# Kernel optimization log

Measured on AMD Instinct MI355X. Metric: run time of the kernel, lower is better.

The kernel has to match this reference:

```python
import jax, jax.numpy as jnp
import numpy as np


def setup_inputs() -> dict:
    key = jax.random.key(0)
    ks = jax.random.split(key, 4)
    B, S, D, H, E = 2, 2048, 1024, 4096, 8
    scale_in = 1.0 / np.sqrt(D)
    scale_h = 1.0 / np.sqrt(H)
    return {
        "x": jax.random.normal(ks[0], (B, S, D), dtype=jnp.float32),
        "Wr": jax.random.normal(ks[1], (E, D), dtype=jnp.float32) * scale_in,
        "br": jnp.zeros((E,), dtype=jnp.float32),
        "W1": jax.random.normal(ks[2], (E, H, D), dtype=jnp.float32) * scale_in,
        "b1": jnp.zeros((E, H), dtype=jnp.float32),
        "W2": jax.random.normal(ks[3], (E, D, H), dtype=jnp.float32) * scale_h,
        "b2": jnp.zeros((E, D), dtype=jnp.float32),
        "top_k": 2,
    }


def reference(x, Wr, br, W1, b1, W2, b2, top_k):
    B, S, D = x.shape
    E = Wr.shape[0]
    x_flat = x.reshape(-1, D)                                   # [N, D]
    # Router: top-k logits, softmax over the selected k values only
    logits = x_flat @ Wr.T + br                                 # [N, E]
    top_vals, top_idx = jax.lax.top_k(logits, top_k)            # [N, k]
    gates = jax.nn.softmax(top_vals, axis=-1)                   # [N, k]
    # Per-expert combine weight: gate_e[n, e] = sum_k gates[n, k] * 1[top_idx[n,k]==e]
    gate_e = jnp.einsum("nk,nke->ne", gates,
                        jax.nn.one_hot(top_idx, E, dtype=x.dtype))  # [N, E]
    # Dense all-expert MLP (grouped GEMM), then masked combine. Same math as
    # the per-expert gather/scatter loop: unselected experts get zero gate.
    h = jax.nn.relu(jnp.einsum("nd,ehd->neh", x_flat, W1) + b1)     # [N, E, H]
    y = jnp.einsum("neh,edh->ned", h, W2) + b2                      # [N, E, D]
    out = jnp.einsum("ned,ne->nd", y, gate_e)                       # [N, D]
    return out.reshape(B, S, D)
```

## Files before the change

### kernel.cpp

```cpp
#include <hip/hip_runtime.h>
#include <hip/hip_bf16.h>
#include <stdint.h>

#define N_TOK 4096
#define D_ 1024
#define H_ 4096
#define E_ 8
#define NSLOT (N_TOK*2)
#define BM 128
#define BN 128
#define BK 32
#define MAXT 72
#define BM2 256
#define BN2 256
#define BK2 32
#define MAXT2 40

typedef __attribute__((ext_vector_type(8))) short short8;
typedef __attribute__((ext_vector_type(4))) float floatx4;
typedef unsigned int u32;

__device__ __forceinline__ unsigned short f2bf(float f){
    union { float f; unsigned int u; } c; c.f = f;
    unsigned int u = c.u;
    unsigned int r = (u + 0x7fffu + ((u >> 16) & 1u)) >> 16;
    return (unsigned short)r;
}

__device__ __forceinline__ void async16(const void* g, void* l){
    __builtin_amdgcn_global_load_lds(
        (const __attribute__((address_space(1))) u32*)g,
        (__attribute__((address_space(3))) u32*)l, 16, 0, 0);
}

__device__ __forceinline__ void sb(){ __builtin_amdgcn_sched_barrier(0); }
__device__ __forceinline__ void barrier_only(){ sb(); __builtin_amdgcn_s_barrier(); sb(); }

__global__ __launch_bounds__(256) void cvt_kernel(
    const float* __restrict__ src, unsigned short* __restrict__ dst, int n4)
{
    int stride = gridDim.x * 256;
    for (int i = blockIdx.x * 256 + threadIdx.x; i < n4; i += stride){
        float4 v = ((const float4*)src)[i];
        ushort4 o; o.x=f2bf(v.x); o.y=f2bf(v.y); o.z=f2bf(v.z); o.w=f2bf(v.w);
        ((ushort4*)dst)[i] = o;
    }
}

__global__ __launch_bounds__(256) void router_kernel(
    const float* __restrict__ x, const float* __restrict__ Wr,
    const float* __restrict__ br, int* __restrict__ topIdx,
    float* __restrict__ topGate)
{
    int n = blockIdx.x * 4 + (threadIdx.x >> 6);
    int lane = threadIdx.x & 63;
    const float4* xp = (const float4*)(x + (size_t)n * D_);
    float acc[E_];
#pragma unroll
    for (int e = 0; e < E_; e++) acc[e] = 0.f;
#pragma unroll
    for (int j = 0; j < 4; j++){
        int idx = j * 64 + lane;
        float4 xv = xp[idx];
#pragma unroll
        for (int e = 0; e < E_; e++){
            float4 wv = ((const float4*)(Wr + (size_t)e * D_))[idx];
            acc[e] += xv.x*wv.x + xv.y*wv.y + xv.z*wv.z + xv.w*wv.w;
        }
    }
#pragma unroll
    for (int e = 0; e < E_; e++){
        float v = acc[e];
        for (int off = 32; off > 0; off >>= 1) v += __shfl_xor(v, off, 64);
        acc[e] = v;
    }
    if (lane == 0){
        float best = -1e30f, second = -1e30f; int bi = 0, si = 0;
#pragma unroll
        for (int e = 0; e < E_; e++){
            float v = acc[e] + br[e];
            if (v > best){ second = best; si = bi; best = v; bi = e; }
            else if (v > second){ second = v; si = e; }
        }
        float e1 = __expf(second - best);
        float denom = 1.f + e1;
        topIdx[n*2+0] = bi;  topIdx[n*2+1] = si;
        topGate[n*2+0] = 1.f/denom;  topGate[n*2+1] = e1/denom;
    }
}

__global__ __launch_bounds__(256) void hist_kernel(
    const int* __restrict__ topIdx, int* __restrict__ hdr)
{
    __shared__ int c[E_];
    int t = threadIdx.x;
    if (t < E_) c[t] = 0;
    __syncthreads();
    int e = topIdx[blockIdx.x * 256 + t];
    atomicAdd(&c[e], 1);
    __syncthreads();
    if (t < E_) hdr[256 + blockIdx.x * E_ + t] = c[t];
}

__global__ __launch_bounds__(64) void scan2_kernel(int* __restrict__ hdr)
{
    __shared__ int cnt[32 * E_];
    __shared__ int tot[E_];
    __shared__ int offs[E_ + 1];
    int t = threadIdx.x;
    for (int i = t; i < 32 * E_; i += 64) cnt[i] = hdr[256 + i];
    __syncthreads();
    if (t < E_){
        int s = 0;
        for (int b = 0; b < 32; b++) s += cnt[b * E_ + t];
        tot[t] = s;
    }
    __syncthreads();
    if (t == 0){
        int o = 0;
        for (int e = 0; e < E_; e++){ offs[e] = o; o += tot[e]; }
        offs[E_] = o;
    }
    __syncthreads();
    if (t < E_ + 1) hdr[16 + t] = offs[t];
    if (t < E_){
        int run = offs[t];
        for (int b = 0; b < 32; b++){ hdr[512 + b * E_ + t] = run; run += cnt[b * E_ + t]; }
    }
    if (t == 0){
        int tn = 0;
        for (int e = 0; e < E_; e++){
            int nt = (tot[e] + BM - 1) >> 7;
            for (int i = 0; i < nt; i++){ hdr[32 + tn] = e; hdr[112 + tn] = offs[e] + (i << 7); tn++; }
        }
        for (; tn < MAXT; tn++){ hdr[32 + tn] = -1; hdr[112 + tn] = 0; }
        int t2 = 0;
        for (int e = 0; e < E_; e++){
            int nt = (tot[e] + BM2 - 1) >> 8;
            for (int i = 0; i < nt; i++){ hdr[768 + t2] = e; hdr[808 + t2] = offs[e] + (i << 8); t2++; }
        }
        for (; t2 < MAXT2; t2++){ hdr[768 + t2] = -1; hdr[808 + t2] = 0; }
    }
}

__global__ __launch_bounds__(256) void pos_kernel(
    const int* __restrict__ topIdx, const float* __restrict__ topGate,
    const int* __restrict__ hdr, int* __restrict__ posOf,
    int* __restrict__ rowTok, float* __restrict__ rowGate)
{
    __shared__ int c[E_];
    int t = threadIdx.x;
    if (t < E_) c[t] = 0;
    __syncthreads();
    int slot = blockIdx.x * 256 + t;
    int e = topIdx[slot];
    int r = atomicAdd(&c[e], 1);
    int pos = hdr[512 + blockIdx.x * E_ + e] + r;
    posOf[slot] = pos;
    rowTok[pos] = slot >> 1;
    rowGate[pos] = topGate[slot];
}

__global__ __launch_bounds__(256) void copy_kernel(
    const float* __restrict__ x, const int* __restrict__ posOf,
    unsigned short* __restrict__ xg)
{
    int slot = blockIdx.x * 4 + (threadIdx.x >> 6);
    int lane = threadIdx.x & 63;
    int n = slot >> 1;
    int pos = posOf[slot];
    const float4* xp = (const float4*)(x + (size_t)n * D_);
    ushort4* op = (ushort4*)(xg + (size_t)pos * D_);
#pragma unroll
    for (int j = 0; j < 4; j++){
        float4 v = xp[j * 64 + lane];
        ushort4 o; o.x=f2bf(v.x); o.y=f2bf(v.y); o.z=f2bf(v.z); o.w=f2bf(v.w);
        op[j * 64 + lane] = o;
    }
}

template<int MODE>
__global__ __launch_bounds__(512, 2) void moe_gemm2(
    const unsigned short* __restrict__ A, int Ktot,
    const unsigned short* __restrict__ Wbase, size_t wStride,
    const float* __restrict__ biasBase, int biasStride,
    const int* __restrict__ hdr,
    const int* __restrict__ rowTok, const float* __restrict__ rowGate,
    unsigned short* __restrict__ hout, float* __restrict__ out)
{
    int nwg  = gridDim.x * gridDim.y * gridDim.z;
    int orig = (blockIdx.z * gridDim.y + blockIdx.y) * gridDim.x + blockIdx.x;
    int xcd = orig & 7, loc = orig >> 3;
    int q8 = nwg >> 3, r8 = nwg & 7;
    int wgid = (xcd < r8 ? xcd * (q8 + 1) : r8 * (q8 + 1) + (xcd - r8) * q8) + loc;
    int bx = wgid % gridDim.x;
    int tt = wgid / gridDim.x;
    int by = tt % gridDim.y;
    int bz = tt / gridDim.y;

    int e = hdr[768 + bx];
    if (e < 0) return;
    int rowBase = hdr[808 + bx];
    int validRows = hdr[16 + e + 1] - rowBase;

    int kChunk = Ktot / gridDim.z;
    int kStart = bz * kChunk;
    int nIter  = kChunk / BK2;

    __shared__ __align__(16) unsigned short As[4][BM2 * BK2];
    __shared__ __align__(16) unsigned short Bs[4][BN2 * BK2];

    const int tid  = threadIdx.x;
    const int lane = tid & 63, wave = tid >> 6;
    const int wm = wave >> 2, wn = wave & 3;
    const int l16 = lane & 15, quad = lane >> 4;

    const unsigned short* Wexp = Wbase + (size_t)e * wStride + (size_t)(by * BN2) * Ktot;

    u32 aOff[2], bOff[2], lOff[2];
#pragma unroll
    for (int i = 0; i < 2; i++){
        int s = i * 512 + tid;
        int rr = s >> 2, gst = s & 3;
        int gsrc = gst ^ ((rr >> 1) & 3);
        int ar = rowBase + rr; ar = ar < (NSLOT - 1) ? ar : (NSLOT - 1);
        aOff[i] = (u32)ar * (u32)Ktot + (u32)(gsrc * 8);
        bOff[i] = (u32)rr * (u32)Ktot + (u32)(gsrc * 8);
        lOff[i] = (u32)(s * 16);
    }

    floatx4 acc[8][4];
#pragma unroll
    for (int mi = 0; mi < 8; mi++)
#pragma unroll
        for (int ni = 0; ni < 4; ni++)
            acc[mi][ni] = (floatx4){0.f, 0.f, 0.f, 0.f};

    const int pg    = quad ^ ((l16 >> 1) & 3);
    const int aFrag = (wm * 128 + l16) * 32 + pg * 8;
    const int bFrag = (wn * 64  + l16) * 32 + pg * 8;

    auto issueA = [&](int kt){
        u32 k0 = (u32)(kStart + kt * BK2);
#pragma unroll
        for (int i = 0; i < 2; i++)
            async16(A + aOff[i] + k0, (char*)As[kt & 3] + lOff[i]);
    };
    auto issueB = [&](int kt){
        u32 k0 = (u32)(kStart + kt * BK2);
#pragma unroll
        for (int i = 0; i < 2; i++)
            async16(Wexp + bOff[i] + k0, (char*)Bs[kt & 3] + lOff[i]);
    };

    issueA(0); issueB(0);
    if (1 < nIter){ issueA(1); issueB(1); }
    if (2 < nIter){ issueA(2); issueB(2); }
    sb();
    if (nIter >= 3) asm volatile("s_waitcnt vmcnt(8)");
    else            asm volatile("s_waitcnt vmcnt(0)");
    barrier_only();

    for (int kt = 0; kt < nIter; kt++){
        const unsigned short* Ab = As[kt & 3];
        const unsigned short* Bb = Bs[kt & 3];

        short8 af[8];
#pragma unroll
        for (int mi = 0; mi < 8; mi++)
            af[mi] = *(const short8*)(Ab + aFrag + mi * 512);
        short8 bf0 = *(const short8*)(Bb + bFrag);
        short8 bf1 = *(const short8*)(Bb + bFrag + 512);
        if (kt + 3 < nIter) issueA(kt + 3);
        sb();
        __builtin_amdgcn_s_barrier();
        asm volatile("s_waitcnt lgkmcnt(0)");
        sb();
        __builtin_amdgcn_s_setprio(1);
#pragma unroll
        for (int mi = 0; mi < 8; mi++)
            acc[mi][0] = __builtin_amdgcn_mfma_f32_16x16x32_bf16(af[mi], bf0, acc[mi][0], 0, 0, 0);
#pragma unroll
        for (int mi = 0; mi < 8; mi++)
            acc[mi][1] = __builtin_amdgcn_mfma_f32_16x16x32_bf16(af[mi], bf1, acc[mi][1], 0, 0, 0);
        __builtin_amdgcn_s_setprio(0);
        barrier_only();

        short8 bf2 = *(const short8*)(Bb + bFrag + 1024);
        short8 bf3 = *(const short8*)(Bb + bFrag + 1536);
        if (kt + 3 < nIter) issueB(kt + 3);
        sb();
        __builtin_amdgcn_s_barrier();
        asm volatile("s_waitcnt lgkmcnt(0)");
        sb();
        __builtin_amdgcn_s_setprio(1);
#pragma unroll
        for (int mi = 0; mi < 8; mi++)
            acc[mi][2] = __builtin_amdgcn_mfma_f32_16x16x32_bf16(af[mi], bf2, acc[mi][2], 0, 0, 0);
#pragma unroll
        for (int mi = 0; mi < 8; mi++)
            acc[mi][3] = __builtin_amdgcn_mfma_f32_16x16x32_bf16(af[mi], bf3, acc[mi][3], 0, 0, 0);
        __builtin_amdgcn_s_setprio(0);
        sb();
        if (kt + 3 < nIter)       asm volatile("s_waitcnt vmcnt(8)");
        else if (kt + 3 == nIter) asm volatile("s_waitcnt vmcnt(4)");
        else if (kt + 2 == nIter) asm volatile("s_waitcnt vmcnt(0)");
        barrier_only();
    }

    bool addB = (MODE == 1) || (bz == 0);
    const float* biasE = biasBase + (size_t)e * biasStride + by * BN2;
    float biasv[4];
#pragma unroll
    for (int ni = 0; ni < 4; ni++)
        biasv[ni] = addB ? biasE[wn * 64 + ni * 16 + l16] : 0.f;

#pragma unroll
    for (int mi = 0; mi < 8; mi++){
#pragma unroll
        for (int r2 = 0; r2 < 4; r2++){
            int rl = wm * 128 + mi * 16 + quad * 4 + r2;
            if (rl >= validRows) continue;
            int grow = rowBase + rl;
            int tok = 0; float gate = 0.f;
            if (MODE == 2){ tok = rowTok[grow]; gate = rowGate[grow]; }
#pragma unroll
            for (int ni = 0; ni < 4; ni++){
                int gcol = by * BN2 + wn * 64 + ni * 16 + l16;
                float v = acc[mi][ni][r2] + biasv[ni];
                if (MODE == 1){
                    v = v > 0.f ? v : 0.f;
                    hout[(size_t)grow * H_ + gcol] = f2bf(v);
                } else {
                    atomicAdd(out + (size_t)tok * D_ + gcol, gate * v);
                }
            }
        }
    }
}

template<int MODE, bool BF16B>
__global__ __launch_bounds__(256) void moe_gemm(
    const unsigned short* __restrict__ A, int Ktot,
    const void* __restrict__ Wbase, size_t wStride,
    const float* __restrict__ biasBase, int biasStride,
    const int* __restrict__ hdr,
    const int* __restrict__ rowTok, const float* __restrict__ rowGate,
    unsigned short* __restrict__ hout, float* __restrict__ out)
{
    int gid = blockIdx.y * gridDim.x + blockIdx.x;
    int per = gridDim.x * 8;
    int g = gid / per, rr = gid % per;
    int by = g * 8 + (rr & 7);
    int bx = rr >> 3;

    int e = hdr[32 + bx];
    if (e < 0) return;
    int rowBase = hdr[112 + bx];
    int validRows = hdr[16 + e + 1] - rowBase;

    int kChunk = Ktot / gridDim.z;
    int kStart = blockIdx.z * kChunk;

    __shared__ __align__(16) unsigned short As[2][BM * BK];
    __shared__ __align__(16) unsigned short BsH[BF16B ? 2 * BN * BK : 1];
    __shared__ __align__(16) float BsF[BF16B ? 1 : BN * BK];

    const float* biasE = biasBase + (size_t)e * biasStride + by * BN;

    const int tid  = threadIdx.x;
    const int lane = tid & 63, wave = tid >> 6;
    const int wm = wave & 1, wn = wave >> 1;
    const int l16 = lane & 15, quad = lane >> 4;

    floatx4 acc[4][4];
#pragma unroll
    for (int mi = 0; mi < 4; mi++)
#pragma unroll
        for (int ni = 0; ni < 4; ni++)
            acc[mi][ni] = (floatx4){0.f,0.f,0.f,0.f};

    if (BF16B){
        const unsigned short* Wexp = (const unsigned short*)Wbase
            + (size_t)e * wStride + (size_t)(by * BN) * Ktot;
        size_t aOff[2], bOff[2];
        int    lOff[2];
#pragma unroll
        for (int i = 0; i < 2; i++){
            int s = i * 256 + tid;
            int r = s >> 2, gst = s & 3;
            int gsrc = gst ^ ((r >> 1) & 3);
            int ar = rowBase + r;
            ar = ar < (NSLOT - 1) ? ar : (NSLOT - 1);
            aOff[i] = (size_t)ar * Ktot + gsrc * 8;
            bOff[i] = (size_t)r  * Ktot + gsrc * 8;
            lOff[i] = s * 16;
        }
#pragma unroll
        for (int i = 0; i < 2; i++){
            async16(A    + aOff[i] + kStart, (char*)As[0]  + lOff[i]);
            async16(Wexp + bOff[i] + kStart, (char*)BsH    + lOff[i]);
        }
        int nIter = kChunk / BK;
        for (int it = 0; it < nIter; it++){
            __syncthreads();
            int p = it & 1;
            if (it + 1 < nIter){
                int kn = kStart + (it + 1) * BK;
#pragma unroll
                for (int i = 0; i < 2; i++){
                    async16(A    + aOff[i] + kn, (char*)As[p ^ 1] + lOff[i]);
                    async16(Wexp + bOff[i] + kn, (char*)BsH + (p ^ 1) * (BN * BK * 2) + lOff[i]);
                }
            }
            short8 af[4], bfr[4];
#pragma unroll
            for (int mi = 0; mi < 4; mi++){
                int r = wm*64 + mi*16 + l16;
                int gq = quad ^ ((r >> 1) & 3);
                af[mi] = *(const short8*)(As[p] + r * BK + gq * 8);
            }
#pragma unroll
            for (int ni = 0; ni < 4; ni++){
                int n = wn*64 + ni*16 + l16;
                int gq = quad ^ ((n >> 1) & 3);
                bfr[ni] = *(const short8*)(BsH + p * (BN * BK) + n * BK + gq * 8);
            }
#pragma unroll
            for (int mi = 0; mi < 4; mi++)
#pragma unroll
                for (int ni = 0; ni < 4; ni++)
                    acc[mi][ni] = __builtin_amdgcn_mfma_f32_16x16x32_bf16(
                        af[mi], bfr[ni], acc[mi][ni], 0, 0, 0);
        }
    } else {
        const float* Wexp = (const float*)Wbase
            + (size_t)e * wStride + (size_t)(by * BN) * Ktot;
        int aS[2], aRow[2], aCol[2];
#pragma unroll
        for (int i = 0; i < 2; i++){
            int s = i * 256 + tid;
            aS[i] = s;
            int r = rowBase + (s >> 2);
            aRow[i] = r < (NSLOT - 1) ? r : (NSLOT - 1);
            aCol[i] = (s & 3) * 8;
        }
        int bS[4], bRow[4], bCol[4];
#pragma unroll
        for (int i = 0; i < 4; i++){
            int s = i * 256 + tid;
            bS[i] = s;
            int r = s >> 3, c = s & 7;
            bRow[i] = r;
            bCol[i] = (c ^ (r & 7)) * 4;
        }
        for (int k0 = kStart; k0 < kStart + kChunk; k0 += BK){
#pragma unroll
            for (int i = 0; i < 2; i++)
                async16(A + (size_t)aRow[i] * Ktot + k0 + aCol[i], (char*)As[0] + aS[i] * 16);
#pragma unroll
            for (int i = 0; i < 4; i++)
                async16(Wexp + (size_t)bRow[i] * Ktot + k0 + bCol[i], (char*)BsF + bS[i] * 16);
            __syncthreads();
            short8 af[4], bfr[4];
#pragma unroll
            for (int mi = 0; mi < 4; mi++)
                af[mi] = *(const short8*)(As[0] + (wm*64 + mi*16 + l16) * BK + quad * 8);
#pragma unroll
            for (int ni = 0; ni < 4; ni++){
                int n = wn*64 + ni*16 + l16;
                int g0 = (2*quad)     ^ (n & 7);
                int g1 = (2*quad + 1) ^ (n & 7);
                float4 u0 = *(const float4*)(BsF + n * BK + g0 * 4);
                float4 u1 = *(const float4*)(BsF + n * BK + g1 * 4);
                union { short8 s; __hip_bfloat162 h[4]; } u;
                u.h[0] = __float22bfloat162_rn(make_float2(u0.x, u0.y));
                u.h[1] = __float22bfloat162_rn(make_float2(u0.z, u0.w));
                u.h[2] = __float22bfloat162_rn(make_float2(u1.x, u1.y));
                u.h[3] = __float22bfloat162_rn(make_float2(u1.z, u1.w));
                bfr[ni] = u.s;
            }
#pragma unroll
            for (int mi = 0; mi < 4; mi++)
#pragma unroll
                for (int ni = 0; ni < 4; ni++)
                    acc[mi][ni] = __builtin_amdgcn_mfma_f32_16x16x32_bf16(
                        af[mi], bfr[ni], acc[mi][ni], 0, 0, 0);
            __syncthreads();
        }
    }

    bool addB = (MODE == 1) || (blockIdx.z == 0);
#pragma unroll
    for (int mi = 0; mi < 4; mi++){
#pragma unroll
        for (int r = 0; r < 4; r++){
            int rl = wm*64 + mi*16 + quad*4 + r;
            if (rl >= validRows) continue;
            int grow = rowBase + rl;
            int   tok  = 0;
            float gate = 0.f;
            if (MODE == 2){ tok = rowTok[grow]; gate = rowGate[grow]; }
#pragma unroll
            for (int ni = 0; ni < 4; ni++){
                int lcol = wn*64 + ni*16 + l16;
                int gcol = by * BN + lcol;
                float v = acc[mi][ni][r] + (addB ? biasE[lcol] : 0.f);
                if (MODE == 1){
                    v = v > 0.f ? v : 0.f;
                    hout[(size_t)grow * H_ + gcol] = f2bf(v);
                } else {
                    atomicAdd(out + (size_t)tok * D_ + gcol, gate * v);
                }
            }
        }
    }
}

extern "C" void kernel_launch(void* const* d_in, const int* in_sizes, int n_in,
                              void* d_out, int out_size, void* d_ws, size_t ws_size,
                              hipStream_t stream)
{
    (void)in_sizes; (void)n_in;
    const float* x  = (const float*)d_in[0];
    const float* Wr = (const float*)d_in[1];
    const float* br = (const float*)d_in[2];
    const float* W1 = (const float*)d_in[3];
    const float* b1 = (const float*)d_in[4];
    const float* W2 = (const float*)d_in[5];
    const float* b2 = (const float*)d_in[6];
    float* out = (float*)d_out;

    char* ws = (char*)d_ws;
    int*   hdr     = (int*)ws;
    int*   topIdx  = (int*)  (ws + 4096);
    float* topGate = (float*)(ws + 36864);
    int*   posOf   = (int*)  (ws + 69632);
    int*   rowTok  = (int*)  (ws + 102400);
    float* rowGate = (float*)(ws + 135168);
    unsigned short* xg   = (unsigned short*)(ws + 262144);
    unsigned short* hbuf = (unsigned short*)(ws + 17039360);
    unsigned short* w1b  = (unsigned short*)(ws + 84148224);
    unsigned short* w2b  = (unsigned short*)(ws + 151257088);
    const bool full = ws_size >= 218365952ull;

    hipMemsetAsync(d_out, 0, (size_t)out_size * sizeof(float), stream);

    router_kernel<<<N_TOK/4, 256, 0, stream>>>(x, Wr, br, topIdx, topGate);
    hist_kernel<<<32, 256, 0, stream>>>(topIdx, hdr);
    scan2_kernel<<<1, 64, 0, stream>>>(hdr);
    pos_kernel<<<32, 256, 0, stream>>>(topIdx, topGate, hdr, posOf, rowTok, rowGate);
    copy_kernel<<<NSLOT/4, 256, 0, stream>>>(x, posOf, xg);

    if (full){
        cvt_kernel<<<2048, 256, 0, stream>>>(W1, w1b, (E_*H_*D_)/4);
        cvt_kernel<<<2048, 256, 0, stream>>>(W2, w2b, (E_*D_*H_)/4);
        moe_gemm2<1><<<dim3(MAXT2, H_/BN2, 1), 512, 0, stream>>>(
            xg, D_, w1b, (size_t)H_ * D_, b1, H_, hdr, rowTok, rowGate, hbuf, nullptr);
        moe_gemm2<2><<<dim3(MAXT2, D_/BN2, 4), 512, 0, stream>>>(
            hbuf, H_, w2b, (size_t)D_ * H_, b2, D_, hdr, rowTok, rowGate, nullptr, out);
    } else {
        moe_gemm<1,false><<<dim3(MAXT, H_/BN, 1), 256, 0, stream>>>(
            xg, D_, W1, (size_t)H_ * D_, b1, H_, hdr, rowTok, rowGate, hbuf, nullptr);
        moe_gemm<2,false><<<dim3(MAXT, D_/BN, 2), 256, 0, stream>>>(
            hbuf, H_, W2, (size_t)D_ * H_, b2, D_, hdr, rowTok, rowGate, nullptr, out);
    }
}
```

Measured before the change: 666.4 us.

## Replace 4-stage async pipeline with 2-stage double buffer and raise occupancy

The MoE GEMM main loop drops its 4-deep async LDS prefetch, which relied on hand-placed vmcnt waits and split barriers. In its place is a simple double buffer: one __syncthreads per K step, then all A and B fragments are loaded and 32 MFMAs issued in one block. This halves LDS use, and the launch bound is raised from 2 to 4 blocks so more workgroups can be resident per CU. The cost is a shallower prefetch, a full barrier with vmcnt(0) every step, and a tighter register budget. That budget may not fit the 128-float accumulator tile without spilling.

```diff
diff --git a/kernel.cpp b/kernel.cpp
--- a/kernel.cpp
+++ b/kernel.cpp
@@ -33,9 +33,6 @@
         (__attribute__((address_space(3))) u32*)l, 16, 0, 0);
 }
 
-__device__ __forceinline__ void sb(){ __builtin_amdgcn_sched_barrier(0); }
-__device__ __forceinline__ void barrier_only(){ sb(); __builtin_amdgcn_s_barrier(); sb(); }
-
 __global__ __launch_bounds__(256) void cvt_kernel(
     const float* __restrict__ src, unsigned short* __restrict__ dst, int n4)
 {
@@ -180,7 +177,7 @@
 }
 
 template<int MODE>
-__global__ __launch_bounds__(512, 2) void moe_gemm2(
+__global__ __launch_bounds__(512, 4) void moe_gemm2(
     const unsigned short* __restrict__ A, int Ktot,
     const unsigned short* __restrict__ Wbase, size_t wStride,
     const float* __restrict__ biasBase, int biasStride,
@@ -207,8 +204,8 @@
     int kStart = bz * kChunk;
     int nIter  = kChunk / BK2;
 
-    __shared__ __align__(16) unsigned short As[4][BM2 * BK2];
-    __shared__ __align__(16) unsigned short Bs[4][BN2 * BK2];
+    __shared__ __align__(16) unsigned short As[2][BM2 * BK2];
+    __shared__ __align__(16) unsigned short Bs[2][BN2 * BK2];
 
     const int tid  = threadIdx.x;
     const int lane = tid & 63, wave = tid >> 6;
@@ -240,72 +237,38 @@
     const int aFrag = (wm * 128 + l16) * 32 + pg * 8;
     const int bFrag = (wn * 64  + l16) * 32 + pg * 8;
 
-    auto issueA = [&](int kt){
-        u32 k0 = (u32)(kStart + kt * BK2);
-#pragma unroll
-        for (int i = 0; i < 2; i++)
-            async16(A + aOff[i] + k0, (char*)As[kt & 3] + lOff[i]);
-    };
-    auto issueB = [&](int kt){
-        u32 k0 = (u32)(kStart + kt * BK2);
-#pragma unroll
-        for (int i = 0; i < 2; i++)
-            async16(Wexp + bOff[i] + k0, (char*)Bs[kt & 3] + lOff[i]);
-    };
-
-    issueA(0); issueB(0);
-    if (1 < nIter){ issueA(1); issueB(1); }
-    if (2 < nIter){ issueA(2); issueB(2); }
-    sb();
-    if (nIter >= 3) asm volatile("s_waitcnt vmcnt(8)");
-    else            asm volatile("s_waitcnt vmcnt(0)");
-    barrier_only();
-
-    for (int kt = 0; kt < nIter; kt++){
-        const unsigned short* Ab = As[kt & 3];
-        const unsigned short* Bb = Bs[kt & 3];
-
-        short8 af[8];
+#pragma unroll
+    for (int i = 0; i < 2; i++){
+        async16(A    + aOff[i] + kStart, (char*)As[0] + lOff[i]);
+        async16(Wexp + bOff[i] + kStart, (char*)Bs[0] + lOff[i]);
+    }
+
+    for (int it = 0; it < nIter; it++){
+        __syncthreads();
+        int p = it & 1;
+        if (it + 1 < nIter){
+            int kn = kStart + (it + 1) * BK2;
+#pragma unroll
+            for (int i = 0; i < 2; i++){
+                async16(A    + aOff[i] + kn, (char*)As[p ^ 1] + lOff[i]);
+                async16(Wexp + bOff[i] + kn, (char*)Bs[p ^ 1] + lOff[i]);
+            }
+        }
+        short8 af[8], bfr[4];
 #pragma unroll
         for (int mi = 0; mi < 8; mi++)
-            af[mi] = *(const short8*)(Ab + aFrag + mi * 512);
-        short8 bf0 = *(const short8*)(Bb + bFrag);
-        short8 bf1 = *(const short8*)(Bb + bFrag + 512);
-        if (kt + 3 < nIter) issueA(kt + 3);
-        sb();
-        __builtin_amdgcn_s_barrier();
-        asm volatile("s_waitcnt lgkmcnt(0)");
-        sb();
+            af[mi] = *(const short8*)(As[p] + aFrag + mi * 512);
+#pragma unroll
+        for (int ni = 0; ni < 4; ni++)
+            bfr[ni] = *(const short8*)(Bs[p] + bFrag + ni * 512);
         __builtin_amdgcn_s_setprio(1);
 #pragma unroll
         for (int mi = 0; mi < 8; mi++)
-            acc[mi][0] = __builtin_amdgcn_mfma_f32_16x16x32_bf16(af[mi], bf0, acc[mi][0], 0, 0, 0);
-#pragma unroll
-        for (int mi = 0; mi < 8; mi++)
-            acc[mi][1] = __builtin_amdgcn_mfma_f32_16x16x32_bf16(af[mi], bf1, acc[mi][1], 0, 0, 0);
+#pragma unroll
+            for (int ni = 0; ni < 4; ni++)
+                acc[mi][ni] = __builtin_amdgcn_mfma_f32_16x16x32_bf16(
+                    af[mi], bfr[ni], acc[mi][ni], 0, 0, 0);
         __builtin_amdgcn_s_setprio(0);
-        barrier_only();
-
-        short8 bf2 = *(const short8*)(Bb + bFrag + 1024);
-        short8 bf3 = *(const short8*)(Bb + bFrag + 1536);
-        if (kt + 3 < nIter) issueB(kt + 3);
-        sb();
-        __builtin_amdgcn_s_barrier();
-        asm volatile("s_waitcnt lgkmcnt(0)");
-        sb();
-        __builtin_amdgcn_s_setprio(1);
-#pragma unroll
-        for (int mi = 0; mi < 8; mi++)
-            acc[mi][2] = __builtin_amdgcn_mfma_f32_16x16x32_bf16(af[mi], bf2, acc[mi][2], 0, 0, 0);
-#pragma unroll
-        for (int mi = 0; mi < 8; mi++)
-            acc[mi][3] = __builtin_amdgcn_mfma_f32_16x16x32_bf16(af[mi], bf3, acc[mi][3], 0, 0, 0);
-        __builtin_amdgcn_s_setprio(0);
-        sb();
-        if (kt + 3 < nIter)       asm volatile("s_waitcnt vmcnt(8)");
-        else if (kt + 3 == nIter) asm volatile("s_waitcnt vmcnt(4)");
-        else if (kt + 2 == nIter) asm volatile("s_waitcnt vmcnt(0)");
-        barrier_only();
     }
 
     bool addB = (MODE == 1) || (bz == 0);
```

Result: slower. 2.468 ms (+270.4%).
